# Kernel optimization log

Measured on AMD Instinct MI355X. Metric: run time of the kernel, lower is better.

## Reference

```python
import jax, jax.numpy as jnp
import numpy as np

S = 3136        # tokens (56x56 patch grid, single image segment -> full attention)
H = 16          # num_heads
D = 80          # head_dim (= head_dim_ori = PADDING_HEAD_DIM)
HID = H * D     # 1280
SCALE = 1.0 / float(np.sqrt(D))  # qkScale = 1/sqrt(head_dim_ori)


def _rope_tables(s, d, base=10000.0):
    # rotate_half style: cos/sin of shape [s, d], duplicated over the two halves
    half = d // 2
    inv_freq = 1.0 / (base ** (np.arange(0, half, dtype=np.float32) / half))
    freqs = np.outer(np.arange(s, dtype=np.float32), inv_freq)  # [s, d/2]
    emb = np.concatenate([freqs, freqs], axis=-1)               # [s, d]
    return jnp.asarray(np.cos(emb)), jnp.asarray(np.sin(emb))


def setup_inputs() -> dict:
    key = jax.random.key(0)
    ks = jax.random.split(key, 6)
    cos, sin = _rope_tables(S, D)
    return {
        "hidden_states": jax.random.normal(ks[0], (S, HID), jnp.float32),
        "x_norm": jax.random.normal(ks[1], (S, HID), jnp.float32),
        "qkv_w": jax.random.normal(ks[2], (3 * HID, HID), jnp.float32) * 0.02,
        "qkv_b": jax.random.normal(ks[3], (3 * HID,), jnp.float32) * 0.02,
        "proj_w": jax.random.normal(ks[4], (HID, HID), jnp.float32) * 0.02,
        "proj_b": jax.random.normal(ks[5], (HID,), jnp.float32) * 0.02,
        "cos": cos,
        "sin": sin,
    }


def _rotate_half(x):
    x1, x2 = jnp.split(x, 2, axis=-1)
    return jnp.concatenate([-x2, x1], axis=-1)


def reference(hidden_states, x_norm, qkv_w, qkv_b, proj_w, proj_b, cos, sin):
    # fused QKV linear (transposeB=True) + split into q,k,v along last dim
    qkv = x_norm @ qkv_w.T + qkv_b                      # [S, 3*HID]
    q, k, v = jnp.split(qkv, 3, axis=-1)                # each [S, HID]
    q = q.reshape(S, H, D)
    k = k.reshape(S, H, D)
    v = v.reshape(S, H, D)
    # inline RoPE on q and k (rotate_half over full head_dim)
    c = cos[:, None, :]; s = sin[:, None, :]           # [S,1,D]
    q = q * c + _rotate_half(q) * s
    k = k * c + _rotate_half(k) * s
    # full self-attention (PA_ENCODER, single segment = seq_len S)
    scores = jnp.einsum('shd,thd->hst', q, k) * SCALE   # [H,S,S]
    probs = jax.nn.softmax(scores, axis=-1)
    attn = jnp.einsum('hst,thd->shd', probs, v)         # [S,H,D]
    attn = attn.reshape(S, HID)
    # output projection + residual add
    out = attn @ proj_w.T + proj_b
    return hidden_states + out
```

## Files before the change

### kernel.cpp

```cpp
#include <hip/hip_runtime.h>
#include <hip/hip_bf16.h>

#define S_   3136
#define H_   16
#define D_   80
#define DP_  96
#define HID_ 1280

typedef short  bf16x8 __attribute__((ext_vector_type(8)));
typedef short  bf16x4 __attribute__((ext_vector_type(4)));
typedef float  f32x4  __attribute__((ext_vector_type(4)));

__device__ __forceinline__ float b2f(unsigned short u) {
    union { unsigned int i; float f; } c;
    c.i = ((unsigned int)u) << 16;
    return c.f;
}
__device__ __forceinline__ unsigned short f2b(float f) {
    union { unsigned int i; float f; } c;
    c.f = f;
    unsigned int x = c.i;
    unsigned int lsb = (x >> 16) & 1u;
    x += 0x7fffu + lsb;
    return (unsigned short)(x >> 16);
}
__device__ __forceinline__ unsigned int cvt_pk_bf16(float lo, float hi) {
    unsigned int r;
    asm("v_cvt_pk_bf16_f32 %0, %1, %2" : "=v"(r) : "v"(lo), "v"(hi));
    return r;
}
__device__ __forceinline__ float exp2_hw(float x) {
    float r;
    asm("v_exp_f32 %0, %1" : "=v"(r) : "v"(x));
    return r;
}

typedef const void __attribute__((address_space(1))) GAS;
typedef void __attribute__((address_space(3))) LAS;
__device__ __forceinline__ void gl16(const void* g, void* l) {
    __builtin_amdgcn_global_load_lds((GAS*)g, (LAS*)l, 16, 0, 0);
}

#define N4_X 1003520
#define N4_Q 1228800
#define N4_P 409600

__global__ __launch_bounds__(256)
void cast3_kernel(const float* __restrict__ x0, unsigned short* __restrict__ y0,
                  const float* __restrict__ x1, unsigned short* __restrict__ y1,
                  const float* __restrict__ x2, unsigned short* __restrict__ y2)
{
    int i = blockIdx.x * 256 + threadIdx.x;
    const float* src; unsigned short* dst;
    if (i < N4_X)               { src = x0; dst = y0; }
    else if (i < N4_X + N4_Q)   { src = x1; dst = y1; i -= N4_X; }
    else if (i < N4_X + N4_Q + N4_P) { src = x2; dst = y2; i -= N4_X + N4_Q; }
    else return;
    float4 v = ((const float4*)src)[i];
    ushort4 o;
    o.x = f2b(v.x); o.y = f2b(v.y); o.z = f2b(v.z); o.w = f2b(v.w);
    ((ushort4*)dst)[i] = o;
}

#define ASTR 40

__global__ __launch_bounds__(256)
void qkv_mfma_kernel(const unsigned short* __restrict__ Ab,
                     const unsigned short* __restrict__ Wb,
                     const float* __restrict__ bias,
                     unsigned short* __restrict__ qo, unsigned short* __restrict__ ko,
                     unsigned short* __restrict__ vtb)
{
    __shared__ __align__(16) short As[2][128][ASTR];
    __shared__ __align__(16) short Bs[2][128][ASTR];
    int m0 = blockIdx.x * 128;
    int n0 = blockIdx.y * 128;
    int t = threadIdx.x;
    int wave = t >> 6, lane = t & 63, lq = lane & 15, quad = lane >> 4;
    int wr = wave >> 1, wc = wave & 1;

    int r0  = t >> 2;
    int r1  = r0 + 64;
    int kc0 = (t & 3) << 3;
    const unsigned short* pa0 = Ab + (size_t)min(m0 + r0, S_ - 1) * HID_ + kc0;
    const unsigned short* pa1 = Ab + (size_t)min(m0 + r1, S_ - 1) * HID_ + kc0;
    const unsigned short* pb0 = Wb + (size_t)(n0 + r0) * HID_ + kc0;
    const unsigned short* pb1 = Wb + (size_t)(n0 + r1) * HID_ + kc0;

    const bf16x8* afp[2][4]; const bf16x8* bfp[2][4];
    #pragma unroll
    for (int s = 0; s < 2; ++s)
        #pragma unroll
        for (int i = 0; i < 4; ++i) {
            afp[s][i] = (const bf16x8*)&As[s][wr * 64 + i * 16 + lq][quad * 8];
            bfp[s][i] = (const bf16x8*)&Bs[s][wc * 64 + i * 16 + lq][quad * 8];
        }

    f32x4 acc[4][4];
    #pragma unroll
    for (int i = 0; i < 4; ++i)
        #pragma unroll
        for (int j = 0; j < 4; ++j) acc[i][j] = (f32x4){0.f, 0.f, 0.f, 0.f};

    bf16x8 va[2][2], vb[2][2];
    #pragma unroll
    for (int s = 0; s < 2; ++s) {
        va[s][0] = *(const bf16x8*)(pa0 + s * 32);
        va[s][1] = *(const bf16x8*)(pa1 + s * 32);
        vb[s][0] = *(const bf16x8*)(pb0 + s * 32);
        vb[s][1] = *(const bf16x8*)(pb1 + s * 32);
    }

    for (int kt = 0; kt < HID_; kt += 64) {
        __syncthreads();
        #pragma unroll
        for (int s = 0; s < 2; ++s) {
            *(bf16x8*)&As[s][r0][kc0] = va[s][0];
            *(bf16x8*)&As[s][r1][kc0] = va[s][1];
            *(bf16x8*)&Bs[s][r0][kc0] = vb[s][0];
            *(bf16x8*)&Bs[s][r1][kc0] = vb[s][1];
        }
        __syncthreads();
        if (kt + 64 < HID_) {
            #pragma unroll
            for (int s = 0; s < 2; ++s) {
                va[s][0] = *(const bf16x8*)(pa0 + kt + 64 + s * 32);
                va[s][1] = *(const bf16x8*)(pa1 + kt + 64 + s * 32);
                vb[s][0] = *(const bf16x8*)(pb0 + kt + 64 + s * 32);
                vb[s][1] = *(const bf16x8*)(pb1 + kt + 64 + s * 32);
            }
        }
        #pragma unroll
        for (int s = 0; s < 2; ++s) {
            bf16x8 af[4], bfr[4];
            #pragma unroll
            for (int i = 0; i < 4; ++i) af[i]  = *afp[s][i];
            #pragma unroll
            for (int j = 0; j < 4; ++j) bfr[j] = *bfp[s][j];
            #pragma unroll
            for (int i = 0; i < 4; ++i)
                #pragma unroll
                for (int j = 0; j < 4; ++j)
                    acc[i][j] = __builtin_amdgcn_mfma_f32_16x16x32_bf16(af[i], bfr[j], acc[i][j], 0, 0, 0);
        }
    }

    #pragma unroll
    for (int i = 0; i < 4; ++i)
        #pragma unroll
        for (int j = 0; j < 4; ++j)
            #pragma unroll
            for (int reg = 0; reg < 4; ++reg) {
                int row = m0 + wr * 64 + i * 16 + quad * 4 + reg;
                if (row >= S_) continue;
                int col = n0 + wc * 64 + j * 16 + lq;
                float val = acc[i][j][reg] + bias[col];
                int which = col / HID_;
                int rem   = col - which * HID_;
                int h     = rem / D_;
                int d     = rem - h * D_;
                if (which == 0)      qo[((size_t)h * S_ + row) * D_ + d] = f2b(val);
                else if (which == 1) ko[((size_t)h * S_ + row) * D_ + d] = f2b(val);
                else                 vtb[((size_t)h * D_ + d) * S_ + row] = f2b(val);
            }
}

__global__ __launch_bounds__(256)
void proj_mfma_kernel(const unsigned short* __restrict__ Ab,
                      const unsigned short* __restrict__ Wb,
                      const float* __restrict__ bias, const float* __restrict__ hidden,
                      float* __restrict__ out)
{
    __shared__ __align__(16) short As[4][64][ASTR];
    __shared__ __align__(16) short Bs[4][64][ASTR];
    int m0 = blockIdx.x * 64;
    int n0 = blockIdx.y * 64;
    int t = threadIdx.x;
    int wave = t >> 6, lane = t & 63, lq = lane & 15, quad = lane >> 4;
    int wr = wave >> 1, wc = wave & 1;

    int r  = t >> 2;
    int kc0 = (t & 3) << 3;
    const unsigned short* pa = Ab + (size_t)(m0 + r) * HID_ + kc0;
    const unsigned short* pb = Wb + (size_t)(n0 + r) * HID_ + kc0;

    const bf16x8* afp[4][2]; const bf16x8* bfp[4][2];
    #pragma unroll
    for (int s = 0; s < 4; ++s)
        #pragma unroll
        for (int i = 0; i < 2; ++i) {
            afp[s][i] = (const bf16x8*)&As[s][wr * 32 + i * 16 + lq][quad * 8];
            bfp[s][i] = (const bf16x8*)&Bs[s][wc * 32 + i * 16 + lq][quad * 8];
        }

    f32x4 acc[2][2];
    #pragma unroll
    for (int i = 0; i < 2; ++i)
        #pragma unroll
        for (int j = 0; j < 2; ++j) acc[i][j] = (f32x4){0.f, 0.f, 0.f, 0.f};

    bf16x8 va[4], vb[4];
    #pragma unroll
    for (int s = 0; s < 4; ++s) {
        va[s] = *(const bf16x8*)(pa + s * 32);
        vb[s] = *(const bf16x8*)(pb + s * 32);
    }

    for (int kt = 0; kt < HID_; kt += 128) {
        __syncthreads();
        #pragma unroll
        for (int s = 0; s < 4; ++s) {
            *(bf16x8*)&As[s][r][kc0] = va[s];
            *(bf16x8*)&Bs[s][r][kc0] = vb[s];
        }
        __syncthreads();
        if (kt + 128 < HID_) {
            #pragma unroll
            for (int s = 0; s < 4; ++s) {
                va[s] = *(const bf16x8*)(pa + kt + 128 + s * 32);
                vb[s] = *(const bf16x8*)(pb + kt + 128 + s * 32);
            }
        }
        #pragma unroll
        for (int s = 0; s < 4; ++s) {
            bf16x8 af[2], bfr[2];
            #pragma unroll
            for (int i = 0; i < 2; ++i) af[i]  = *afp[s][i];
            #pragma unroll
            for (int j = 0; j < 2; ++j) bfr[j] = *bfp[s][j];
            #pragma unroll
            for (int i = 0; i < 2; ++i)
                #pragma unroll
                for (int j = 0; j < 2; ++j)
                    acc[i][j] = __builtin_amdgcn_mfma_f32_16x16x32_bf16(af[i], bfr[j], acc[i][j], 0, 0, 0);
        }
    }

    #pragma unroll
    for (int i = 0; i < 2; ++i)
        #pragma unroll
        for (int j = 0; j < 2; ++j)
            #pragma unroll
            for (int reg = 0; reg < 4; ++reg) {
                int row = m0 + wr * 32 + i * 16 + quad * 4 + reg;
                int col = n0 + wc * 32 + j * 16 + lq;
                out[(size_t)row * HID_ + col] =
                    acc[i][j][reg] + bias[col] + hidden[(size_t)row * HID_ + col];
            }
}

__global__ __launch_bounds__(256)
void rope_kernel(const unsigned short* __restrict__ q, const unsigned short* __restrict__ k,
                 const float* __restrict__ cost, const float* __restrict__ sint,
                 unsigned short* __restrict__ qb, unsigned short* __restrict__ kb)
{
    const float QSCALE = 0.11180339887498949f * 1.4426950408889634f;
    int idx = blockIdx.x * 256 + threadIdx.x;
    const int total = H_ * S_ * 5;
    if (idx >= total) return;
    int j  = idx % 5;
    int hs = idx / 5;
    int s  = hs % S_;
    int d0 = j * 8;
    const unsigned short* qp = q + (size_t)hs * D_ + d0;
    const unsigned short* kp = k + (size_t)hs * D_ + d0;
    unsigned short* qo = qb + (size_t)hs * DP_ + d0;
    unsigned short* ko = kb + (size_t)hs * DP_ + d0;
    const float* cp = cost + s * D_ + d0;
    const float* sp = sint + s * D_ + d0;

    bf16x8 q1 = *(const bf16x8*)(qp);
    bf16x8 q2 = *(const bf16x8*)(qp + 40);
    bf16x8 k1 = *(const bf16x8*)(kp);
    bf16x8 k2 = *(const bf16x8*)(kp + 40);
    f32x4 c1[2] = { *(const f32x4*)(cp),      *(const f32x4*)(cp + 4)  };
    f32x4 c2[2] = { *(const f32x4*)(cp + 40), *(const f32x4*)(cp + 44) };
    f32x4 s1[2] = { *(const f32x4*)(sp),      *(const f32x4*)(sp + 4)  };
    f32x4 s2[2] = { *(const f32x4*)(sp + 40), *(const f32x4*)(sp + 44) };

    bf16x8 oq1, oq2, ok1, ok2;
    #pragma unroll
    for (int e = 0; e < 8; ++e) {
        float cc1 = c1[e >> 2][e & 3], ss1 = s1[e >> 2][e & 3];
        float cc2 = c2[e >> 2][e & 3], ss2 = s2[e >> 2][e & 3];
        float x1 = b2f((unsigned short)q1[e]), x2 = b2f((unsigned short)q2[e]);
        oq1[e] = (short)f2b((x1 * cc1 - x2 * ss1) * QSCALE);
        oq2[e] = (short)f2b((x2 * cc2 + x1 * ss2) * QSCALE);
        x1 = b2f((unsigned short)k1[e]); x2 = b2f((unsigned short)k2[e]);
        ok1[e] = (short)f2b(x1 * cc1 - x2 * ss1);
        ok2[e] = (short)f2b(x2 * cc2 + x1 * ss2);
    }
    *(bf16x8*)(qo)      = oq1;
    *(bf16x8*)(qo + 40) = oq2;
    *(bf16x8*)(ko)      = ok1;
    *(bf16x8*)(ko + 40) = ok2;
    if (j == 0) {
        uint4 z = {0u, 0u, 0u, 0u};
        *(uint4*)(qo + 80) = z;
        *(uint4*)(qo + 88) = z;
        *(uint4*)(ko + 80) = z;
        *(uint4*)(ko + 88) = z;
    }
}

#define KBUF_ 16384
#define VBUF_ 10240
#define BUF_  26624

__global__ __launch_bounds__(256, 3)
void attn_kernel(const unsigned short* __restrict__ Qb,
                 const unsigned short* __restrict__ Kb,
                 const unsigned short* __restrict__ Vtb,
                 unsigned short* __restrict__ attnb)
{
    __shared__ __align__(16) unsigned char smem[2 * BUF_];

    int h   = blockIdx.y;
    int qb0 = blockIdx.x * 64;
    int t      = threadIdx.x;
    int wave   = t >> 6;
    int lane   = t & 63;
    int lq     = lane & 15;
    int quad   = lane >> 4;
    int qh     = wave & 1;
    int stripe = wave >> 1;
    int Q0     = qb0 + qh * 32;
    int swz    = (lq & 7) << 4;

    bf16x8 qf[2][3];
    #pragma unroll
    for (int qt = 0; qt < 2; ++qt)
        #pragma unroll
        for (int kc = 0; kc < 3; ++kc)
            qf[qt][kc] = *(const bf16x8*)(Qb + ((size_t)h * S_ + Q0 + qt * 16 + lq) * DP_ + kc * 32 + quad * 8);

    f32x4 O[2][5];
    #pragma unroll
    for (int qt = 0; qt < 2; ++qt)
        #pragma unroll
        for (int dt = 0; dt < 5; ++dt) O[qt][dt] = (f32x4){0.f, 0.f, 0.f, 0.f};
    float l_acc[2] = {0.f, 0.f};

    const unsigned char* kS[4]; int kD[4];
    #pragma unroll
    for (int ii = 0; ii < 4; ++ii) {
        int i  = wave * 4 + ii;
        int rl = i * 4 + (lane >> 4);
        kS[ii] = (const unsigned char*)(Kb + ((size_t)h * S_ + rl) * DP_)
               + (((lane & 15) * 16) ^ ((rl & 7) << 4));
        kD[ii] = i * 1024;
    }
    const unsigned char* vS[3]; int vD[3];
    int nv = (wave < 2) ? 3 : 2;
    #pragma unroll
    for (int jj = 0; jj < 3; ++jj) {
        int j = (jj < 2) ? (wave + jj * 4) : (8 + wave);
        int d = j * 8 + (lane >> 3);
        vS[jj] = (const unsigned char*)(Vtb + (size_t)(h * D_ + d) * S_)
               + (((lane & 7) * 16) ^ ((d & 7) << 4));
        vD[jj] = KBUF_ + j * 1024;
    }

    #define STAGE(bufoff, rr)                                                   \
        do {                                                                    \
            size_t kadv = (size_t)(rr) * (64 * DP_ * 2);                        \
            size_t vadv = (size_t)(rr) * 128;                                   \
            _Pragma("unroll")                                                   \
            for (int ii = 0; ii < 4; ++ii)                                      \
                gl16(kS[ii] + kadv, smem + (bufoff) + kD[ii]);                  \
            _Pragma("unroll")                                                   \
            for (int jj = 0; jj < 3; ++jj)                                      \
                if (jj < nv) gl16(vS[jj] + vadv, smem + (bufoff) + vD[jj]);     \
        } while (0)

    STAGE(0, 0);
    asm volatile("s_waitcnt vmcnt(0)" ::: "memory");
    __syncthreads();

    int cur = 0;
    for (int r = 0; r < 49; ++r) {
        if (r < 48) STAGE(cur ^ BUF_, r + 1);

        const unsigned char* Kbase = smem + cur;
        const unsigned char* Vbase = Kbase + KBUF_;

        f32x4 sc[2][2];
        __builtin_amdgcn_s_setprio(1);
        #pragma unroll
        for (int kt = 0; kt < 2; ++kt) {
            const unsigned char* kbp = Kbase + (stripe * 32 + kt * 16 + lq) * 256;
            bf16x8 kf0 = *(const bf16x8*)(kbp + ((  0 + quad * 16) ^ swz));
            bf16x8 kf1 = *(const bf16x8*)(kbp + (( 64 + quad * 16) ^ swz));
            bf16x8 kf2 = *(const bf16x8*)(kbp + ((128 + quad * 16) ^ swz));
            #pragma unroll
            for (int qt = 0; qt < 2; ++qt) {
                f32x4 a = (f32x4){0.f, 0.f, 0.f, 0.f};
                a = __builtin_amdgcn_mfma_f32_16x16x32_bf16(kf0, qf[qt][0], a, 0, 0, 0);
                a = __builtin_amdgcn_mfma_f32_16x16x32_bf16(kf1, qf[qt][1], a, 0, 0, 0);
                a = __builtin_amdgcn_mfma_f32_16x16x32_bf16(kf2, qf[qt][2], a, 0, 0, 0);
                sc[qt][kt] = a;
            }
        }
        __builtin_amdgcn_s_setprio(0);

        union PaU { bf16x8 v8; unsigned int d[4]; } pa[2];
        #pragma unroll
        for (int qt = 0; qt < 2; ++qt) {
            float e00 = exp2_hw(sc[qt][0][0]), e01 = exp2_hw(sc[qt][0][1]);
            float e02 = exp2_hw(sc[qt][0][2]), e03 = exp2_hw(sc[qt][0][3]);
            float e10 = exp2_hw(sc[qt][1][0]), e11 = exp2_hw(sc[qt][1][1]);
            float e12 = exp2_hw(sc[qt][1][2]), e13 = exp2_hw(sc[qt][1][3]);
            l_acc[qt] += ((e00 + e01) + (e02 + e03)) + ((e10 + e11) + (e12 + e13));
            pa[qt].d[0] = cvt_pk_bf16(e00, e01);
            pa[qt].d[1] = cvt_pk_bf16(e02, e03);
            pa[qt].d[2] = cvt_pk_bf16(e10, e11);
            pa[qt].d[3] = cvt_pk_bf16(e12, e13);
        }

        __builtin_amdgcn_s_setprio(1);
        #pragma unroll
        for (int dt = 0; dt < 5; ++dt) {
            const unsigned char* vbp = Vbase + (dt * 16 + lq) * 128;
            union { bf16x8 v8; bf16x4 v4[2]; } vv;
            vv.v4[0] = *(const bf16x4*)(vbp + ((stripe * 64 +      quad * 8) ^ swz));
            vv.v4[1] = *(const bf16x4*)(vbp + ((stripe * 64 + 32 + quad * 8) ^ swz));
            #pragma unroll
            for (int qt = 0; qt < 2; ++qt)
                O[qt][dt] = __builtin_amdgcn_mfma_f32_16x16x32_bf16(pa[qt].v8, vv.v8, O[qt][dt], 0, 0, 0);
        }
        __builtin_amdgcn_s_setprio(0);

        asm volatile("s_waitcnt vmcnt(0)" ::: "memory");
        __syncthreads();
        cur ^= BUF_;
    }
    #undef STAGE

    float lr[2];
    #pragma unroll
    for (int qt = 0; qt < 2; ++qt) {
        float l = l_acc[qt];
        l += __shfl_xor(l, 16);
        l += __shfl_xor(l, 32);
        lr[qt] = l;
    }
    f32x4* Of = (f32x4*)smem;
    float* Lf = (float*)(smem + 20480);
    if (stripe == 1) {
        #pragma unroll
        for (int qt = 0; qt < 2; ++qt) {
            #pragma unroll
            for (int dt = 0; dt < 5; ++dt)
                Of[((qh * 2 + qt) * 5 + dt) * 64 + lane] = O[qt][dt];
            if (lane < 16) Lf[(qh * 2 + qt) * 16 + lane] = lr[qt];
        }
    }
    __syncthreads();
    if (stripe == 0) {
        #pragma unroll
        for (int qt = 0; qt < 2; ++qt) {
            float ltot = lr[qt] + Lf[(qh * 2 + qt) * 16 + lq];
            #pragma unroll
            for (int dt = 0; dt < 5; ++dt)
                O[qt][dt] += Of[((qh * 2 + qt) * 5 + dt) * 64 + lane];
            #pragma unroll
            for (int reg = 0; reg < 4; ++reg) {
                float l = __shfl(ltot, quad * 4 + reg, 16);
                float linv = 1.0f / l;
                int s = Q0 + qt * 16 + quad * 4 + reg;
                unsigned short* orow = attnb + (size_t)s * HID_ + h * D_;
                #pragma unroll
                for (int dt = 0; dt < 5; ++dt)
                    orow[dt * 16 + lq] = f2b(O[qt][dt][reg] * linv);
            }
        }
    }
}

extern "C" void kernel_launch(void* const* d_in, const int* in_sizes, int n_in,
                              void* d_out, int out_size, void* d_ws, size_t ws_size,
                              hipStream_t stream)
{
    const float* hidden = (const float*)d_in[0];
    const float* x_norm = (const float*)d_in[1];
    const float* qkv_w  = (const float*)d_in[2];
    const float* qkv_b  = (const float*)d_in[3];
    const float* proj_w = (const float*)d_in[4];
    const float* proj_b = (const float*)d_in[5];
    const float* cost   = (const float*)d_in[6];
    const float* sint   = (const float*)d_in[7];
    float* out = (float*)d_out;

    unsigned short* w      = (unsigned short*)d_ws;
    unsigned short* qbuf   = w;
    unsigned short* kbuf   = qbuf + 4014080;
    unsigned short* vtb    = kbuf + 4014080;
    unsigned short* kbb    = vtb + 4064256;
    unsigned short* xb     = kbb + 4816896;
    unsigned short* wqkvb  = xb + 4014080;
    unsigned short* wprojb = wqkvb + 4915200;
    unsigned short* qbb    = wqkvb;
    unsigned short* abuf   = qbuf;

    cast3_kernel<<<(N4_X + N4_Q + N4_P + 255) / 256, 256, 0, stream>>>(
        x_norm, xb, qkv_w, wqkvb, proj_w, wprojb);

    qkv_mfma_kernel<<<dim3(25, 30), 256, 0, stream>>>(xb, wqkvb, qkv_b, qbuf, kbuf, vtb);
    rope_kernel<<<(H_ * S_ * 5 + 255) / 256, 256, 0, stream>>>(qbuf, kbuf, cost, sint, qbb, kbb);
    attn_kernel<<<dim3(S_ / 64, H_), 256, 0, stream>>>(qbb, kbb, vtb, abuf);
    proj_mfma_kernel<<<dim3(49, 20), 256, 0, stream>>>(abuf, wprojb, proj_b, hidden, out);
}
```

Baseline: 301.4 us.

## Triple-buffer K/V tiles in LDS with two-stage prefetch in attention

```diff
diff --git a/kernel.cpp b/kernel.cpp
--- a/kernel.cpp
+++ b/kernel.cpp
@@ -307,13 +307,13 @@
 #define VBUF_ 10240
 #define BUF_  26624
 
-__global__ __launch_bounds__(256, 3)
+__global__ __launch_bounds__(256, 2)
 void attn_kernel(const unsigned short* __restrict__ Qb,
                  const unsigned short* __restrict__ Kb,
                  const unsigned short* __restrict__ Vtb,
                  unsigned short* __restrict__ attnb)
 {
-    __shared__ __align__(16) unsigned char smem[2 * BUF_];
+    __shared__ __align__(16) unsigned char smem[3 * BUF_];
 
     int h   = blockIdx.y;
     int qb0 = blockIdx.x * 64;
@@ -373,67 +373,72 @@
                 if (jj < nv) gl16(vS[jj] + vadv, smem + (bufoff) + vD[jj]);     \
         } while (0)
 
-    STAGE(0, 0);
-    asm volatile("s_waitcnt vmcnt(0)" ::: "memory");
+    STAGE(0,    0);
+    STAGE(BUF_, 1);
+    asm volatile("s_waitcnt vmcnt(7)" ::: "memory");
     __syncthreads();
 
-    int cur = 0;
-    for (int r = 0; r < 49; ++r) {
-        if (r < 48) STAGE(cur ^ BUF_, r + 1);
-
-        const unsigned char* Kbase = smem + cur;
-        const unsigned char* Vbase = Kbase + KBUF_;
-
-        f32x4 sc[2][2];
-        __builtin_amdgcn_s_setprio(1);
-        #pragma unroll
-        for (int kt = 0; kt < 2; ++kt) {
-            const unsigned char* kbp = Kbase + (stripe * 32 + kt * 16 + lq) * 256;
-            bf16x8 kf0 = *(const bf16x8*)(kbp + ((  0 + quad * 16) ^ swz));
-            bf16x8 kf1 = *(const bf16x8*)(kbp + (( 64 + quad * 16) ^ swz));
-            bf16x8 kf2 = *(const bf16x8*)(kbp + ((128 + quad * 16) ^ swz));
-            #pragma unroll
-            for (int qt = 0; qt < 2; ++qt) {
-                f32x4 a = (f32x4){0.f, 0.f, 0.f, 0.f};
-                a = __builtin_amdgcn_mfma_f32_16x16x32_bf16(kf0, qf[qt][0], a, 0, 0, 0);
-                a = __builtin_amdgcn_mfma_f32_16x16x32_bf16(kf1, qf[qt][1], a, 0, 0, 0);
-                a = __builtin_amdgcn_mfma_f32_16x16x32_bf16(kf2, qf[qt][2], a, 0, 0, 0);
-                sc[qt][kt] = a;
-            }
-        }
-        __builtin_amdgcn_s_setprio(0);
-
-        union PaU { bf16x8 v8; unsigned int d[4]; } pa[2];
-        #pragma unroll
-        for (int qt = 0; qt < 2; ++qt) {
-            float e00 = exp2_hw(sc[qt][0][0]), e01 = exp2_hw(sc[qt][0][1]);
-            float e02 = exp2_hw(sc[qt][0][2]), e03 = exp2_hw(sc[qt][0][3]);
-            float e10 = exp2_hw(sc[qt][1][0]), e11 = exp2_hw(sc[qt][1][1]);
-            float e12 = exp2_hw(sc[qt][1][2]), e13 = exp2_hw(sc[qt][1][3]);
-            l_acc[qt] += ((e00 + e01) + (e02 + e03)) + ((e10 + e11) + (e12 + e13));
-            pa[qt].d[0] = cvt_pk_bf16(e00, e01);
-            pa[qt].d[1] = cvt_pk_bf16(e02, e03);
-            pa[qt].d[2] = cvt_pk_bf16(e10, e11);
-            pa[qt].d[3] = cvt_pk_bf16(e12, e13);
-        }
-
-        __builtin_amdgcn_s_setprio(1);
-        #pragma unroll
-        for (int dt = 0; dt < 5; ++dt) {
-            const unsigned char* vbp = Vbase + (dt * 16 + lq) * 128;
-            union { bf16x8 v8; bf16x4 v4[2]; } vv;
-            vv.v4[0] = *(const bf16x4*)(vbp + ((stripe * 64 +      quad * 8) ^ swz));
-            vv.v4[1] = *(const bf16x4*)(vbp + ((stripe * 64 + 32 + quad * 8) ^ swz));
-            #pragma unroll
-            for (int qt = 0; qt < 2; ++qt)
-                O[qt][dt] = __builtin_amdgcn_mfma_f32_16x16x32_bf16(pa[qt].v8, vv.v8, O[qt][dt], 0, 0, 0);
-        }
-        __builtin_amdgcn_s_setprio(0);
-
-        asm volatile("s_waitcnt vmcnt(0)" ::: "memory");
-        __syncthreads();
-        cur ^= BUF_;
-    }
+    #define BODY(CUROFF, STGOFF, RVAL)                                          \
+    {                                                                           \
+        int r_ = (RVAL);                                                        \
+        if (r_ <= 46) STAGE((STGOFF), r_ + 2);                                  \
+        const unsigned char* Kbase = smem + (CUROFF);                           \
+        const unsigned char* Vbase = Kbase + KBUF_;                             \
+        f32x4 sc[2][2];                                                         \
+        __builtin_amdgcn_s_setprio(1);                                          \
+        _Pragma("unroll")                                                       \
+        for (int kt = 0; kt < 2; ++kt) {                                        \
+            const unsigned char* kbp = Kbase + (stripe * 32 + kt * 16 + lq) * 256; \
+            bf16x8 kf0 = *(const bf16x8*)(kbp + ((  0 + quad * 16) ^ swz));     \
+            bf16x8 kf1 = *(const bf16x8*)(kbp + (( 64 + quad * 16) ^ swz));     \
+            bf16x8 kf2 = *(const bf16x8*)(kbp + ((128 + quad * 16) ^ swz));     \
+            _Pragma("unroll")                                                   \
+            for (int qt = 0; qt < 2; ++qt) {                                    \
+                f32x4 a = (f32x4){0.f, 0.f, 0.f, 0.f};                          \
+                a = __builtin_amdgcn_mfma_f32_16x16x32_bf16(kf0, qf[qt][0], a, 0, 0, 0); \
+                a = __builtin_amdgcn_mfma_f32_16x16x32_bf16(kf1, qf[qt][1], a, 0, 0, 0); \
+                a = __builtin_amdgcn_mfma_f32_16x16x32_bf16(kf2, qf[qt][2], a, 0, 0, 0); \
+                sc[qt][kt] = a;                                                 \
+            }                                                                   \
+        }                                                                       \
+        __builtin_amdgcn_s_setprio(0);                                          \
+        union PaU { bf16x8 v8; unsigned int d[4]; } pa[2];                      \
+        _Pragma("unroll")                                                       \
+        for (int qt = 0; qt < 2; ++qt) {                                        \
+            float e00 = exp2_hw(sc[qt][0][0]), e01 = exp2_hw(sc[qt][0][1]);     \
+            float e02 = exp2_hw(sc[qt][0][2]), e03 = exp2_hw(sc[qt][0][3]);     \
+            float e10 = exp2_hw(sc[qt][1][0]), e11 = exp2_hw(sc[qt][1][1]);     \
+            float e12 = exp2_hw(sc[qt][1][2]), e13 = exp2_hw(sc[qt][1][3]);     \
+            l_acc[qt] += ((e00 + e01) + (e02 + e03)) + ((e10 + e11) + (e12 + e13)); \
+            pa[qt].d[0] = cvt_pk_bf16(e00, e01);                                \
+            pa[qt].d[1] = cvt_pk_bf16(e02, e03);                                \
+            pa[qt].d[2] = cvt_pk_bf16(e10, e11);                                \
+            pa[qt].d[3] = cvt_pk_bf16(e12, e13);                                \
+        }                                                                       \
+        __builtin_amdgcn_s_setprio(1);                                          \
+        _Pragma("unroll")                                                       \
+        for (int dt = 0; dt < 5; ++dt) {                                        \
+            const unsigned char* vbp = Vbase + (dt * 16 + lq) * 128;            \
+            union { bf16x8 v8; bf16x4 v4[2]; } vv;                              \
+            vv.v4[0] = *(const bf16x4*)(vbp + ((stripe * 64 +      quad * 8) ^ swz)); \
+            vv.v4[1] = *(const bf16x4*)(vbp + ((stripe * 64 + 32 + quad * 8) ^ swz)); \
+            _Pragma("unroll")                                                   \
+            for (int qt = 0; qt < 2; ++qt)                                      \
+                O[qt][dt] = __builtin_amdgcn_mfma_f32_16x16x32_bf16(pa[qt].v8, vv.v8, O[qt][dt], 0, 0, 0); \
+        }                                                                       \
+        __builtin_amdgcn_s_setprio(0);                                          \
+        if (r_ <= 46)      { asm volatile("s_waitcnt vmcnt(7)" ::: "memory"); } \
+        else if (r_ == 47) { asm volatile("s_waitcnt vmcnt(0)" ::: "memory"); } \
+        __syncthreads();                                                        \
+    }
+
+    for (int rr = 0; rr < 16; ++rr) {
+        BODY(0,        2 * BUF_, rr * 3    );
+        BODY(BUF_,     0,        rr * 3 + 1);
+        BODY(2 * BUF_, BUF_,     rr * 3 + 2);
+    }
+    BODY(0, 2 * BUF_, 48);
+    #undef BODY
     #undef STAGE
 
     float lr[2];
```

Result: no change. 298.9 us (-0.8%).
